# Performance work log

Measured on AMD Instinct MI355X. Metric: run time of the kernel, lower is better.

## Reference

```python
import jax, jax.numpy as jnp
import numpy as np

BSZ, SEQ, EMBED = 2, 4096, 1024
NUM_HEADS = 16
HEAD_DIM = EMBED // NUM_HEADS
WINDOW = 256  # attention_window[layer_id]


def setup_inputs() -> dict:
    key = jax.random.key(0)
    ks = jax.random.split(key, 7)
    s = 1.0 / np.sqrt(EMBED)
    return {
        "hidden_states": jax.random.normal(ks[0], (BSZ, SEQ, EMBED), jnp.float32),
        "Wq": jax.random.normal(ks[1], (EMBED, EMBED), jnp.float32) * s,
        "bq": jnp.zeros((EMBED,), jnp.float32),
        "Wk": jax.random.normal(ks[2], (EMBED, EMBED), jnp.float32) * s,
        "bk": jnp.zeros((EMBED,), jnp.float32),
        "Wv": jax.random.normal(ks[3], (EMBED, EMBED), jnp.float32) * s,
        "bv": jnp.zeros((EMBED,), jnp.float32),
    }


def _blocks3(x, nb, w):
    # x: [b, s + 2w, h, d] -> [b, nb, 3w, h, d]; block c sees key blocks c-1, c, c+1
    b = x.shape[0]
    xb = x.reshape(b, nb + 2, w, NUM_HEADS, HEAD_DIM)
    return jnp.concatenate([xb[:, i:i + nb] for i in range(3)], axis=2)


def reference(hidden_states, Wq, bq, Wk, bk, Wv, bv):
    b, s, e = hidden_states.shape
    w = WINDOW
    nb = s // w
    q = (hidden_states @ Wq + bq) * (1.0 / np.sqrt(HEAD_DIM))
    k = hidden_states @ Wk + bk
    v = hidden_states @ Wv + bv
    q = q.reshape(b, nb, w, NUM_HEADS, HEAD_DIM)
    k = k.reshape(b, s, NUM_HEADS, HEAD_DIM)
    v = v.reshape(b, s, NUM_HEADS, HEAD_DIM)
    pad = ((0, 0), (w, w), (0, 0), (0, 0))
    kb = _blocks3(jnp.pad(k, pad), nb, w)  # [b, nb, 3w, h, d]
    vb = _blocks3(jnp.pad(v, pad), nb, w)
    # banded scores: query x in block n attends keys at global pos n*w - w + y
    scores = jnp.einsum('bnxhd,bnyhd->bnhxy', q, kb)  # [b, nb, h, w, 3w]
    x_idx = jnp.arange(w)
    y_idx = jnp.arange(3 * w)
    band = jnp.abs(y_idx[None, :] - x_idx[:, None] - w) <= w  # [w, 3w]
    kpos = jnp.arange(nb)[:, None] * w - w + y_idx[None, :]   # [nb, 3w]
    inb = (kpos >= 0) & (kpos < s)
    mask = band[None, :, :] & inb[:, None, :]                 # [nb, w, 3w]
    scores = jnp.where(mask[None, :, None, :, :], scores, -jnp.inf)
    probs = jax.nn.softmax(scores.astype(jnp.float32), axis=-1).astype(v.dtype)
    attn = jnp.einsum('bnhxy,bnyhd->bnxhd', probs, vb)        # [b, nb, w, h, d]
    return attn.reshape(b, s, e)
```

## Files before the change

kernel.cpp:

```cpp
#include <hip/hip_runtime.h>
#include <stdint.h>

#define SEQ    4096
#define EMBED  1024
#define NHEAD  16
#define HDIM   64
#define WIN    256
#define BSZ    2
#define M_TOT  (BSZ * SEQ)
#define N_QKV  3072
#define N_QK   2048
#define K_DIM  1024
#define LOG2E  1.4426950408889634f

typedef __attribute__((ext_vector_type(8))) __bf16 bf16x8;
typedef __attribute__((ext_vector_type(4))) float  f32x4;

__device__ __forceinline__ unsigned short f2bf(float f) {
  union { float f; unsigned int u; } c; c.f = f;
  unsigned int u = c.u;
  unsigned int r = (u + 0x7FFFu + ((u >> 16) & 1u)) >> 16;
  return (unsigned short)r;
}

__device__ __forceinline__ unsigned int cvt_pk_bf16(float lo, float hi) {
  unsigned int r;
  asm("v_cvt_pk_bf16_f32 %0, %1, %2" : "=v"(r) : "v"(lo), "v"(hi));
  return r;
}

__device__ __forceinline__ void gl2lds16(const void* g, void* l) {
  __builtin_amdgcn_global_load_lds((const __attribute__((address_space(1))) void*)g,
                                   (__attribute__((address_space(3))) void*)l, 16, 0, 0);
}

__global__ __launch_bounds__(256) void cvt_all(const float* __restrict__ in,
                                               unsigned short* __restrict__ out,
                                               const float* __restrict__ Wq,
                                               const float* __restrict__ Wk,
                                               const float* __restrict__ Wv,
                                               unsigned short* __restrict__ Wt) {
  __shared__ float t[32][33];
  int tid = threadIdx.x;
  if (blockIdx.x < 8192) {
    int i = (blockIdx.x * 256 + tid) * 4;
    float4 v = *(const float4*)(in + i);
    ushort4 o;
    o.x = f2bf(v.x); o.y = f2bf(v.y); o.z = f2bf(v.z); o.w = f2bf(v.w);
    *(ushort4*)(out + i) = o;
  } else {
    int wb = blockIdx.x - 8192;
    int z  = wb >> 10;
    int rem = wb & 1023;
    int kb = (rem & 31) * 32, nb = (rem >> 5) * 32;
    const float* W = (z == 0) ? Wq : (z == 1) ? Wk : Wv;
    int tx = tid & 31, ty = tid >> 5;
    for (int it = 0; it < 4; ++it) {
      int k = kb + ty + it * 8;
      t[ty + it * 8][tx] = W[(size_t)k * 1024 + nb + tx];
    }
    __syncthreads();
    for (int it = 0; it < 4; ++it) {
      int n = nb + ty + it * 8;
      Wt[(size_t)(z * 1024 + n) * 1024 + kb + tx] = f2bf(t[tx][ty + it * 8]);
    }
  }
}

__global__ __launch_bounds__(512, 2) void qkv_gemm(const unsigned short* __restrict__ A,
                                                   const unsigned short* __restrict__ Bt,
                                                   const float* __restrict__ bq,
                                                   const float* __restrict__ bk,
                                                   const float* __restrict__ bv,
                                                   unsigned short* __restrict__ C,
                                                   unsigned short* __restrict__ Vt) {
  __shared__ unsigned short As[3][128 * 64];
  __shared__ unsigned short Bs[3][256 * 64];
  int tid  = threadIdx.x;
  int lane = tid & 63, wave = tid >> 6;
  int ln   = lane & 15, quad = lane >> 4;
  int flat = blockIdx.y * 12 + blockIdx.x;
  int swz  = (flat & 7) * 96 + (flat >> 3);
  int m0 = (swz / 12) * 128, n0 = (swz % 12) * 256;
  int wy = wave >> 2, wx = wave & 3;
  f32x4 acc[4][4];
#pragma unroll
  for (int i = 0; i < 4; ++i)
#pragma unroll
    for (int j = 0; j < 4; ++j) acc[i][j] = (f32x4){0.f, 0.f, 0.f, 0.f};

#define STAGE(asW, bsW, kt)                                                      \
  do {                                                                           \
    _Pragma("unroll")                                                            \
    for (int s = 0; s < 2; ++s) {                                                \
      int ch = s * 512 + tid; int r = ch >> 3, c = ch & 7, cg = c ^ (r & 7);     \
      gl2lds16(A + (size_t)(m0 + r) * K_DIM + (size_t)(kt) * 64 + cg * 8,        \
               (asW) + ch * 8);                                                  \
    }                                                                            \
    _Pragma("unroll")                                                            \
    for (int s = 0; s < 4; ++s) {                                                \
      int ch = s * 512 + tid; int r = ch >> 3, c = ch & 7, cg = c ^ (r & 7);     \
      gl2lds16(Bt + (size_t)(n0 + r) * K_DIM + (size_t)(kt) * 64 + cg * 8,       \
               (bsW) + ch * 8);                                                  \
    }                                                                            \
  } while (0)

  unsigned short *pa0 = As[0], *pa1 = As[1], *pa2 = As[2];
  unsigned short *pb0 = Bs[0], *pb1 = Bs[1], *pb2 = Bs[2];

  STAGE(pa0, pb0, 0);
  STAGE(pa1, pb1, 1);
  asm volatile("s_waitcnt vmcnt(6)" ::: "memory");
  __builtin_amdgcn_s_barrier();

  int aBase = wy * 64, bBase = wx * 64;

#pragma unroll 1
  for (int t = 0; t < 16; ++t) {
    if (t < 14) STAGE(pa2, pb2, t + 2);

    bf16x8 af[4][2], bf0[2][2], bf1[2][2];
#pragma unroll
    for (int i2 = 0; i2 < 4; ++i2) {
      int row = aBase + i2 * 16 + ln;
#pragma unroll
      for (int ks = 0; ks < 2; ++ks) {
        int c = (ks * 4 + quad) ^ (row & 7);
        af[i2][ks] = *(const bf16x8*)&pa0[row * 64 + c * 8];
      }
    }
#pragma unroll
    for (int j2 = 0; j2 < 2; ++j2) {
      int row = bBase + j2 * 16 + ln;
#pragma unroll
      for (int ks = 0; ks < 2; ++ks) {
        int c = (ks * 4 + quad) ^ (row & 7);
        bf0[j2][ks] = *(const bf16x8*)&pb0[row * 64 + c * 8];
      }
    }
    __builtin_amdgcn_s_setprio(1);
#pragma unroll
    for (int ks = 0; ks < 2; ++ks)
#pragma unroll
      for (int i2 = 0; i2 < 4; ++i2)
#pragma unroll
        for (int j2 = 0; j2 < 2; ++j2)
          acc[i2][j2] = __builtin_amdgcn_mfma_f32_16x16x32_bf16(af[i2][ks], bf0[j2][ks], acc[i2][j2], 0, 0, 0);
    __builtin_amdgcn_s_setprio(0);
#pragma unroll
    for (int j2 = 0; j2 < 2; ++j2) {
      int row = bBase + 32 + j2 * 16 + ln;
#pragma unroll
      for (int ks = 0; ks < 2; ++ks) {
        int c = (ks * 4 + quad) ^ (row & 7);
        bf1[j2][ks] = *(const bf16x8*)&pb0[row * 64 + c * 8];
      }
    }
    __builtin_amdgcn_s_setprio(1);
#pragma unroll
    for (int ks = 0; ks < 2; ++ks)
#pragma unroll
      for (int i2 = 0; i2 < 4; ++i2)
#pragma unroll
        for (int j2 = 0; j2 < 2; ++j2)
          acc[i2][2 + j2] = __builtin_amdgcn_mfma_f32_16x16x32_bf16(af[i2][ks], bf1[j2][ks], acc[i2][2 + j2], 0, 0, 0);
    __builtin_amdgcn_s_setprio(0);

    if (t < 14) asm volatile("s_waitcnt vmcnt(6)" ::: "memory");
    else        asm volatile("s_waitcnt vmcnt(0)" ::: "memory");
    __builtin_amdgcn_s_barrier();

    unsigned short* tp;
    tp = pa0; pa0 = pa1; pa1 = pa2; pa2 = tp;
    tp = pb0; pb0 = pb1; pb1 = pb2; pb2 = tp;
  }
#undef STAGE

  if (n0 < N_QK) {
#pragma unroll
    for (int j = 0; j < 4; ++j) {
      int n = n0 + wx * 64 + j * 16 + ln;
      float bias, scl;
      if (n < 1024) { bias = bq[n];        scl = 0.125f * LOG2E; }
      else          { bias = bk[n - 1024]; scl = 1.f; }
#pragma unroll
      for (int i = 0; i < 4; ++i) {
        int mb = m0 + wy * 64 + i * 16 + quad * 4;
#pragma unroll
        for (int r = 0; r < 4; ++r) {
          float v = (acc[i][j][r] + bias) * scl;
          C[(size_t)(mb + r) * N_QK + n] = f2bf(v);
        }
      }
    }
  } else {
#pragma unroll
    for (int j = 0; j < 4; ++j) {
      int n  = n0 + wx * 64 + j * 16 + ln;
      int hd = n - 2048;
      float bias = bv[hd];
#pragma unroll
      for (int i = 0; i < 4; ++i) {
        int mb  = m0 + wy * 64 + i * 16 + quad * 4;
        int bb  = mb >> 12;
        int pos = mb & (SEQ - 1);
        ushort4 pk;
        pk.x = f2bf(acc[i][j][0] + bias);
        pk.y = f2bf(acc[i][j][1] + bias);
        pk.z = f2bf(acc[i][j][2] + bias);
        pk.w = f2bf(acc[i][j][3] + bias);
        *(ushort4*)&Vt[((size_t)bb * (NHEAD * HDIM) + hd) * SEQ + pos] = pk;
      }
    }
  }
}

__global__ __launch_bounds__(256) void attn(const unsigned short* __restrict__ qk,
                                            const unsigned short* __restrict__ vtg,
                                            float* __restrict__ out) {
  __shared__ unsigned short Kl[64 * 72];
  __shared__ unsigned short Vl[64 * 72];
  int tid  = threadIdx.x;
  int lane = tid & 63, wave = tid >> 6;
  int ln   = lane & 15, quad = lane >> 4;
  int bx = blockIdx.x;
  int lx = ((bx & 7) << 3) | (bx >> 3);
  int q0 = lx * 64, head = blockIdx.y, b = blockIdx.z;
  size_t baseRow = (size_t)b * SEQ;
  const unsigned short* kptr = qk + 1024;
  const unsigned short* vrow = vtg + ((size_t)(b * NHEAD + head) * HDIM) * SEQ;

  int sy = tid >> 3, sc = tid & 7;
  const unsigned short* kbase = kptr + (baseRow + sy) * (size_t)N_QK + head * HDIM + sc * 8;
  const unsigned short* vbase = vrow + (size_t)sy * SEQ + sc * 8;

  bf16x8 qf[2];
  {
    size_t ro = (baseRow + q0 + wave * 16 + ln) * (size_t)N_QK + head * HDIM + quad * 8;
    qf[0] = *(const bf16x8*)&qk[ro];
    qf[1] = *(const bf16x8*)&qk[ro + 32];
  }

  float l_st = 0.f;
  f32x4 o_acc[4];
  for (int dt = 0; dt < 4; ++dt) o_acc[dt] = (f32x4){0.f, 0.f, 0.f, 0.f};

  int lo = (q0 >= 256) ? 0 : (256 - q0) / 64;
  int hi = (SEQ + 256 - q0) / 64; if (hi > 9) hi = 9;

  uint4 pk0, pk1, pv0, pv1;
#define PREFETCH(KT)                                                        \
  {                                                                         \
    pk0 = *(const uint4*)&kbase[(size_t)(KT) * N_QK];                       \
    pk1 = *(const uint4*)&kbase[(size_t)((KT) + 32) * N_QK];                \
    pv0 = *(const uint4*)&vbase[(KT)];                                      \
    pv1 = *(const uint4*)&vbase[(size_t)32 * SEQ + (KT)];                   \
  }

  PREFETCH(q0 - 256 + lo * 64);

  int srcA = ((lane & 16) << 1) | ln;
  int srcB = srcA + 16;
  bool hiQ = (lane & 32) != 0;

  for (int t = lo; t < hi; ++t) {
    int kt = q0 - 256 + t * 64;
    __syncthreads();
    *(uint4*)&Kl[sy * 72 + sc * 8]        = pk0;
    *(uint4*)&Kl[(sy + 32) * 72 + sc * 8] = pk1;
    *(uint4*)&Vl[sy * 72 + sc * 8]        = pv0;
    *(uint4*)&Vl[(sy + 32) * 72 + sc * 8] = pv1;
    __syncthreads();

    if (t + 1 < hi) { PREFETCH(kt + 64); }

    f32x4 s[4];
    __builtin_amdgcn_s_setprio(1);
    for (int nt = 0; nt < 4; ++nt) {
      bf16x8 kf0 = *(const bf16x8*)&Kl[(nt * 16 + ln) * 72 + quad * 8];
      bf16x8 kf1 = *(const bf16x8*)&Kl[(nt * 16 + ln) * 72 + 32 + quad * 8];
      f32x4 z = (f32x4){0.f, 0.f, 0.f, 0.f};
      z = __builtin_amdgcn_mfma_f32_16x16x32_bf16(kf0, qf[0], z, 0, 0, 0);
      z = __builtin_amdgcn_mfma_f32_16x16x32_bf16(kf1, qf[1], z, 0, 0, 0);
      s[nt] = z;
    }
    __builtin_amdgcn_s_setprio(0);

    if (t == 0 || t == 8) {
      int qq = q0 + wave * 16 + ln;
      for (int nt = 0; nt < 4; ++nt) {
        int kb = kt + nt * 16 + quad * 4 - qq;
        for (int r = 0; r < 4; ++r) {
          int dd = kb + r;
          if (dd < -WIN || dd > WIN) s[nt][r] = -INFINITY;
        }
      }
    }

    float rs = 0.f;
    for (int nt = 0; nt < 4; ++nt)
      for (int r = 0; r < 4; ++r) {
        float p = exp2f(s[nt][r]);
        s[nt][r] = p;
        rs += p;
      }
    l_st += rs;

    unsigned int p01[4], p23[4];
    for (int nt = 0; nt < 4; ++nt) {
      p01[nt] = cvt_pk_bf16(s[nt][0], s[nt][1]);
      p23[nt] = cvt_pk_bf16(s[nt][2], s[nt][3]);
    }

    for (int ks = 0; ks < 2; ++ks) {
      int ntA = 2 * ks, ntB = 2 * ks + 1;
      unsigned int a0 = (unsigned int)__shfl((int)p01[ntA], srcA);
      unsigned int a1 = (unsigned int)__shfl((int)p23[ntA], srcA);
      unsigned int a2 = (unsigned int)__shfl((int)p01[ntA], srcB);
      unsigned int a3 = (unsigned int)__shfl((int)p23[ntA], srcB);
      unsigned int b0 = (unsigned int)__shfl((int)p01[ntB], srcA);
      unsigned int b1 = (unsigned int)__shfl((int)p23[ntB], srcA);
      unsigned int b2 = (unsigned int)__shfl((int)p01[ntB], srcB);
      unsigned int b3 = (unsigned int)__shfl((int)p23[ntB], srcB);
      union { uint4 u; bf16x8 v; } pf;
      pf.u.x = hiQ ? b0 : a0;
      pf.u.y = hiQ ? b1 : a1;
      pf.u.z = hiQ ? b2 : a2;
      pf.u.w = hiQ ? b3 : a3;
      __builtin_amdgcn_s_setprio(1);
      for (int dt = 0; dt < 4; ++dt) {
        bf16x8 vf = *(const bf16x8*)&Vl[(dt * 16 + ln) * 72 + ks * 32 + quad * 8];
        o_acc[dt] = __builtin_amdgcn_mfma_f32_16x16x32_bf16(vf, pf.v, o_acc[dt], 0, 0, 0);
      }
      __builtin_amdgcn_s_setprio(0);
    }
  }

  float l = l_st;
  l += __shfl_xor(l, 16);
  l += __shfl_xor(l, 32);
  float inv = 1.0f / l;
  int qpos = q0 + wave * 16 + ln;
  float* ob = out + (baseRow + qpos) * (size_t)EMBED + head * HDIM + quad * 4;
  for (int dt = 0; dt < 4; ++dt) {
    float4 v;
    v.x = o_acc[dt][0] * inv;
    v.y = o_acc[dt][1] * inv;
    v.z = o_acc[dt][2] * inv;
    v.w = o_acc[dt][3] * inv;
    *(float4*)(ob + dt * 16) = v;
  }
#undef PREFETCH
}

extern "C" void kernel_launch(void* const* d_in, const int* in_sizes, int n_in,
                              void* d_out, int out_size, void* d_ws, size_t ws_size,
                              hipStream_t stream) {
  const float* h  = (const float*)d_in[0];
  const float* Wq = (const float*)d_in[1];
  const float* bq = (const float*)d_in[2];
  const float* Wk = (const float*)d_in[3];
  const float* bk = (const float*)d_in[4];
  const float* Wv = (const float*)d_in[5];
  const float* bv = (const float*)d_in[6];
  float* out = (float*)d_out;

  unsigned short* h_bf  = (unsigned short*)d_ws;
  unsigned short* wt_bf = h_bf + (size_t)M_TOT * K_DIM;
  unsigned short* qk    = wt_bf + (size_t)N_QKV * K_DIM;
  unsigned short* vtg   = qk + (size_t)M_TOT * N_QK;

  cvt_all<<<8192 + 3072, 256, 0, stream>>>(h, h_bf, Wq, Wk, Wv, wt_bf);
  qkv_gemm<<<dim3(12, 64), 512, 0, stream>>>(h_bf, wt_bf, bq, bk, bv, qk, vtg);
  attn<<<dim3(SEQ / 64, NHEAD, BSZ), 256, 0, stream>>>(qk, vtg, out);
}
```

Baseline: 217.3 us.

## Widen QKV GEMM tile to 128x384 with interleaved double-buffer staging; double-prefetch attention

```diff
diff --git a/kernel.cpp b/kernel.cpp
--- a/kernel.cpp
+++ b/kernel.cpp
@@ -74,59 +74,64 @@
                                                    const float* __restrict__ bv,
                                                    unsigned short* __restrict__ C,
                                                    unsigned short* __restrict__ Vt) {
-  __shared__ unsigned short As[3][128 * 64];
-  __shared__ unsigned short Bs[3][256 * 64];
+  __shared__ unsigned short As[2][128 * 64];
+  __shared__ unsigned short Bs[2][384 * 64];
   int tid  = threadIdx.x;
   int lane = tid & 63, wave = tid >> 6;
   int ln   = lane & 15, quad = lane >> 4;
-  int flat = blockIdx.y * 12 + blockIdx.x;
-  int swz  = (flat & 7) * 96 + (flat >> 3);
-  int m0 = (swz / 12) * 128, n0 = (swz % 12) * 256;
+  int flat = blockIdx.y * 8 + blockIdx.x;
+  int swz  = (flat & 7) * 64 + (flat >> 3);
+  int m0 = (swz >> 3) * 128, n0 = (swz & 7) * 384;
   int wy = wave >> 2, wx = wave & 3;
-  f32x4 acc[4][4];
+  f32x4 acc[4][6];
 #pragma unroll
   for (int i = 0; i < 4; ++i)
 #pragma unroll
-    for (int j = 0; j < 4; ++j) acc[i][j] = (f32x4){0.f, 0.f, 0.f, 0.f};
-
-#define STAGE(asW, bsW, kt)                                                      \
+    for (int j = 0; j < 6; ++j) acc[i][j] = (f32x4){0.f, 0.f, 0.f, 0.f};
+
+  int c8 = tid & 7;
+
+#define STG_A(buf, kt)                                                           \
   do {                                                                           \
     _Pragma("unroll")                                                            \
     for (int s = 0; s < 2; ++s) {                                                \
-      int ch = s * 512 + tid; int r = ch >> 3, c = ch & 7, cg = c ^ (r & 7);     \
+      int r = s * 64 + (tid >> 3); int cg = c8 ^ (r & 7);                        \
       gl2lds16(A + (size_t)(m0 + r) * K_DIM + (size_t)(kt) * 64 + cg * 8,        \
-               (asW) + ch * 8);                                                  \
-    }                                                                            \
-    _Pragma("unroll")                                                            \
-    for (int s = 0; s < 4; ++s) {                                                \
-      int ch = s * 512 + tid; int r = ch >> 3, c = ch & 7, cg = c ^ (r & 7);     \
-      gl2lds16(Bt + (size_t)(n0 + r) * K_DIM + (size_t)(kt) * 64 + cg * 8,       \
-               (bsW) + ch * 8);                                                  \
+               &As[buf][r * 64 + c8 * 8]);                                       \
     }                                                                            \
   } while (0)
-
-  unsigned short *pa0 = As[0], *pa1 = As[1], *pa2 = As[2];
-  unsigned short *pb0 = Bs[0], *pb1 = Bs[1], *pb2 = Bs[2];
-
-  STAGE(pa0, pb0, 0);
-  STAGE(pa1, pb1, 1);
+#define STG_B(buf, jreg, kt)                                                     \
+  do {                                                                           \
+    _Pragma("unroll")                                                            \
+    for (int s = 0; s < 2; ++s) {                                                \
+      int r = s * 64 + (tid >> 3); int gr = (jreg) * 128 + r;                    \
+      int cg = c8 ^ (gr & 7);                                                    \
+      gl2lds16(Bt + (size_t)(n0 + gr) * K_DIM + (size_t)(kt) * 64 + cg * 8,      \
+               &Bs[buf][gr * 64 + c8 * 8]);                                      \
+    }                                                                            \
+  } while (0)
+
+  STG_A(0, 0); STG_B(0, 0, 0); STG_B(0, 1, 0); STG_B(0, 2, 0);
+  STG_B(1, 0, 1); STG_B(1, 1, 1); STG_B(1, 2, 1);
   asm volatile("s_waitcnt vmcnt(6)" ::: "memory");
   __builtin_amdgcn_s_barrier();
 
-  int aBase = wy * 64, bBase = wx * 64;
+  int aBase = wy * 64, bBase = wx * 96;
 
 #pragma unroll 1
   for (int t = 0; t < 16; ++t) {
-    if (t < 14) STAGE(pa2, pb2, t + 2);
-
-    bf16x8 af[4][2], bf0[2][2], bf1[2][2];
+    int cur = t & 1;
+    const unsigned short* as = As[cur];
+    const unsigned short* bs = Bs[cur];
+    bf16x8 af[4][2], bf01[2][2], bf23[2][2], bf45[2][2];
+
 #pragma unroll
     for (int i2 = 0; i2 < 4; ++i2) {
       int row = aBase + i2 * 16 + ln;
 #pragma unroll
       for (int ks = 0; ks < 2; ++ks) {
         int c = (ks * 4 + quad) ^ (row & 7);
-        af[i2][ks] = *(const bf16x8*)&pa0[row * 64 + c * 8];
+        af[i2][ks] = *(const bf16x8*)&as[row * 64 + c * 8];
       }
     }
 #pragma unroll
@@ -135,9 +140,11 @@
 #pragma unroll
       for (int ks = 0; ks < 2; ++ks) {
         int c = (ks * 4 + quad) ^ (row & 7);
-        bf0[j2][ks] = *(const bf16x8*)&pb0[row * 64 + c * 8];
-      }
-    }
+        bf01[j2][ks] = *(const bf16x8*)&bs[row * 64 + c * 8];
+      }
+    }
+    if (t < 15) STG_A(cur ^ 1, t + 1);
+    __builtin_amdgcn_s_barrier();
     __builtin_amdgcn_s_setprio(1);
 #pragma unroll
     for (int ks = 0; ks < 2; ++ks)
@@ -145,17 +152,20 @@
       for (int i2 = 0; i2 < 4; ++i2)
 #pragma unroll
         for (int j2 = 0; j2 < 2; ++j2)
-          acc[i2][j2] = __builtin_amdgcn_mfma_f32_16x16x32_bf16(af[i2][ks], bf0[j2][ks], acc[i2][j2], 0, 0, 0);
+          acc[i2][j2] = __builtin_amdgcn_mfma_f32_16x16x32_bf16(af[i2][ks], bf01[j2][ks], acc[i2][j2], 0, 0, 0);
     __builtin_amdgcn_s_setprio(0);
+    __builtin_amdgcn_s_barrier();
+
 #pragma unroll
     for (int j2 = 0; j2 < 2; ++j2) {
       int row = bBase + 32 + j2 * 16 + ln;
 #pragma unroll
       for (int ks = 0; ks < 2; ++ks) {
         int c = (ks * 4 + quad) ^ (row & 7);
-        bf1[j2][ks] = *(const bf16x8*)&pb0[row * 64 + c * 8];
-      }
-    }
+        bf23[j2][ks] = *(const bf16x8*)&bs[row * 64 + c * 8];
+      }
+    }
+    __builtin_amdgcn_s_barrier();
     __builtin_amdgcn_s_setprio(1);
 #pragma unroll
     for (int ks = 0; ks < 2; ++ks)
@@ -163,23 +173,50 @@
       for (int i2 = 0; i2 < 4; ++i2)
 #pragma unroll
         for (int j2 = 0; j2 < 2; ++j2)
-          acc[i2][2 + j2] = __builtin_amdgcn_mfma_f32_16x16x32_bf16(af[i2][ks], bf1[j2][ks], acc[i2][2 + j2], 0, 0, 0);
+          acc[i2][2 + j2] = __builtin_amdgcn_mfma_f32_16x16x32_bf16(af[i2][ks], bf23[j2][ks], acc[i2][2 + j2], 0, 0, 0);
     __builtin_amdgcn_s_setprio(0);
-
+    __builtin_amdgcn_s_barrier();
+
+#pragma unroll
+    for (int j2 = 0; j2 < 2; ++j2) {
+      int row = bBase + 64 + j2 * 16 + ln;
+#pragma unroll
+      for (int ks = 0; ks < 2; ++ks) {
+        int c = (ks * 4 + quad) ^ (row & 7);
+        bf45[j2][ks] = *(const bf16x8*)&bs[row * 64 + c * 8];
+      }
+    }
+    __builtin_amdgcn_s_barrier();
+    __builtin_amdgcn_s_setprio(1);
+#pragma unroll
+    for (int ks = 0; ks < 2; ++ks)
+#pragma unroll
+      for (int i2 = 0; i2 < 4; ++i2)
+        acc[i2][4] = __builtin_amdgcn_mfma_f32_16x16x32_bf16(af[i2][ks], bf45[0][ks], acc[i2][4], 0, 0, 0);
+    __builtin_amdgcn_s_setprio(0);
+    if (t < 14) STG_B(cur, 0, t + 2);
+    __builtin_amdgcn_s_barrier();
+
+    if (t < 14) { STG_B(cur, 1, t + 2); STG_B(cur, 2, t + 2); }
+    __builtin_amdgcn_s_barrier();
+    __builtin_amdgcn_s_setprio(1);
+#pragma unroll
+    for (int ks = 0; ks < 2; ++ks)
+#pragma unroll
+      for (int i2 = 0; i2 < 4; ++i2)
+        acc[i2][5] = __builtin_amdgcn_mfma_f32_16x16x32_bf16(af[i2][ks], bf45[1][ks], acc[i2][5], 0, 0, 0);
+    __builtin_amdgcn_s_setprio(0);
     if (t < 14) asm volatile("s_waitcnt vmcnt(6)" ::: "memory");
     else        asm volatile("s_waitcnt vmcnt(0)" ::: "memory");
     __builtin_amdgcn_s_barrier();
-
-    unsigned short* tp;
-    tp = pa0; pa0 = pa1; pa1 = pa2; pa2 = tp;
-    tp = pb0; pb0 = pb1; pb1 = pb2; pb2 = tp;
-  }
-#undef STAGE
-
-  if (n0 < N_QK) {
-#pragma unroll
-    for (int j = 0; j < 4; ++j) {
-      int n = n0 + wx * 64 + j * 16 + ln;
+  }
+#undef STG_A
+#undef STG_B
+
+#pragma unroll
+  for (int j = 0; j < 6; ++j) {
+    int n = n0 + wx * 96 + j * 16 + ln;
+    if (n < N_QK) {
       float bias, scl;
       if (n < 1024) { bias = bq[n];        scl = 0.125f * LOG2E; }
       else          { bias = bk[n - 1024]; scl = 1.f; }
@@ -192,11 +229,7 @@
           C[(size_t)(mb + r) * N_QK + n] = f2bf(v);
         }
       }
-    }
-  } else {
-#pragma unroll
-    for (int j = 0; j < 4; ++j) {
-      int n  = n0 + wx * 64 + j * 16 + ln;
+    } else {
       int hd = n - 2048;
       float bias = bv[hd];
 #pragma unroll
@@ -248,16 +281,25 @@
   int lo = (q0 >= 256) ? 0 : (256 - q0) / 64;
   int hi = (SEQ + 256 - q0) / 64; if (hi > 9) hi = 9;
 
-  uint4 pk0, pk1, pv0, pv1;
-#define PREFETCH(KT)                                                        \
+  uint4 pkA0, pkA1, pvA0, pvA1;
+  uint4 pkB0, pkB1, pvB0, pvB1;
+#define PREFETCH_A(KT)                                                      \
   {                                                                         \
-    pk0 = *(const uint4*)&kbase[(size_t)(KT) * N_QK];                       \
-    pk1 = *(const uint4*)&kbase[(size_t)((KT) + 32) * N_QK];                \
-    pv0 = *(const uint4*)&vbase[(KT)];                                      \
-    pv1 = *(const uint4*)&vbase[(size_t)32 * SEQ + (KT)];                   \
-  }
-
-  PREFETCH(q0 - 256 + lo * 64);
+    pkA0 = *(const uint4*)&kbase[(size_t)(KT) * N_QK];                      \
+    pkA1 = *(const uint4*)&kbase[(size_t)((KT) + 32) * N_QK];               \
+    pvA0 = *(const uint4*)&vbase[(KT)];                                     \
+    pvA1 = *(const uint4*)&vbase[(size_t)32 * SEQ + (KT)];                  \
+  }
+#define PREFETCH_B(KT)                                                      \
+  {                                                                         \
+    pkB0 = *(const uint4*)&kbase[(size_t)(KT) * N_QK];                      \
+    pkB1 = *(const uint4*)&kbase[(size_t)((KT) + 32) * N_QK];               \
+    pvB0 = *(const uint4*)&vbase[(KT)];                                     \
+    pvB1 = *(const uint4*)&vbase[(size_t)32 * SEQ + (KT)];                  \
+  }
+
+  PREFETCH_A(q0 - 256 + lo * 64);
+  if (lo + 1 < hi) PREFETCH_B(q0 - 256 + (lo + 1) * 64);
 
   int srcA = ((lane & 16) << 1) | ln;
   int srcB = srcA + 16;
@@ -265,14 +307,29 @@
 
   for (int t = lo; t < hi; ++t) {
     int kt = q0 - 256 + t * 64;
-    __syncthreads();
-    *(uint4*)&Kl[sy * 72 + sc * 8]        = pk0;
-    *(uint4*)&Kl[(sy + 32) * 72 + sc * 8] = pk1;
-    *(uint4*)&Vl[sy * 72 + sc * 8]        = pv0;
-    *(uint4*)&Vl[(sy + 32) * 72 + sc * 8] = pv1;
-    __syncthreads();
-
-    if (t + 1 < hi) { PREFETCH(kt + 64); }
+    bool useA = ((t - lo) & 1) == 0;
+
+    asm volatile("s_waitcnt lgkmcnt(0)" ::: "memory");
+    __builtin_amdgcn_sched_barrier(0);
+    __builtin_amdgcn_s_barrier();
+    if (useA) {
+      *(uint4*)&Kl[sy * 72 + sc * 8]        = pkA0;
+      *(uint4*)&Kl[(sy + 32) * 72 + sc * 8] = pkA1;
+      *(uint4*)&Vl[sy * 72 + sc * 8]        = pvA0;
+      *(uint4*)&Vl[(sy + 32) * 72 + sc * 8] = pvA1;
+    } else {
+      *(uint4*)&Kl[sy * 72 + sc * 8]        = pkB0;
+      *(uint4*)&Kl[(sy + 32) * 72 + sc * 8] = pkB1;
+      *(uint4*)&Vl[sy * 72 + sc * 8]        = pvB0;
+      *(uint4*)&Vl[(sy + 32) * 72 + sc * 8] = pvB1;
+    }
+    asm volatile("s_waitcnt lgkmcnt(0)" ::: "memory");
+    __builtin_amdgcn_sched_barrier(0);
+    __builtin_amdgcn_s_barrier();
+
+    if (t + 2 < hi) {
+      if (useA) PREFETCH_A(kt + 128) else PREFETCH_B(kt + 128)
+    }
 
     f32x4 s[4];
     __builtin_amdgcn_s_setprio(1);
@@ -350,7 +407,8 @@
     v.w = o_acc[dt][3] * inv;
     *(float4*)(ob + dt * 16) = v;
   }
-#undef PREFETCH
+#undef PREFETCH_A
+#undef PREFETCH_B
 }
 
 extern "C" void kernel_launch(void* const* d_in, const int* in_sizes, int n_in,
@@ -371,6 +429,6 @@
   unsigned short* vtg   = qk + (size_t)M_TOT * N_QK;
 
   cvt_all<<<8192 + 3072, 256, 0, stream>>>(h, h_bf, Wq, Wk, Wv, wt_bf);
-  qkv_gemm<<<dim3(12, 64), 512, 0, stream>>>(h_bf, wt_bf, bq, bk, bv, qk, vtg);
+  qkv_gemm<<<dim3(8, 64), 512, 0, stream>>>(h_bf, wt_bf, bq, bk, bv, qk, vtg);
   attn<<<dim3(SEQ / 64, NHEAD, BSZ), 256, 0, stream>>>(qk, vtg, out);
 }
```

Result: no change. 214.5 us (-1.3%).
